# Performance work log

Hardware: AMD Instinct MI355X
Metric: run time of the kernel (lower is better)

The kernel has to match this reference:

```python
import jax, jax.numpy as jnp
import numpy as np

SQRT_DK = jnp.sqrt(jnp.float32(128.0))
BN_EPS = 1e-5


def setup_inputs() -> dict:
    key = jax.random.key(0)
    ks = jax.random.split(key, 12)
    B, C, F, Fp, K, O, DK = 4, 64, 20000, 10000, 16, 128, 128
    fea = jax.random.normal(ks[0], (B, C, F), dtype=jnp.float32)
    ring_n = jax.random.randint(ks[1], (B, Fp, K), 0, F, dtype=jnp.int64)
    pool_idx = jnp.sort(jax.random.randint(ks[2], (Fp,), 0, F, dtype=jnp.int64))
    pos_embed = jnp.zeros((1, 1, 1), dtype=jnp.float32)
    s = 1.0 / np.sqrt(C)
    Wk = jax.random.uniform(ks[3], (DK, C), jnp.float32, -s, s)
    bk = jax.random.uniform(ks[4], (DK,), jnp.float32, -s, s)
    Wq = jax.random.uniform(ks[5], (DK, C), jnp.float32, -s, s)
    bq = jax.random.uniform(ks[6], (DK,), jnp.float32, -s, s)
    Wc = jax.random.uniform(ks[7], (O, C), jnp.float32, -s, s)
    bc = jax.random.uniform(ks[8], (O,), jnp.float32, -s, s)
    gamma = jnp.ones((O,), jnp.float32)
    beta = jnp.zeros((O,), jnp.float32)
    return {"fea": fea, "ring_n": ring_n, "pool_idx": pool_idx, "pos_embed": pos_embed,
            "Wk": Wk, "bk": bk, "Wq": Wq, "bq": bq, "Wc": Wc, "bc": bc,
            "gamma": gamma, "beta": beta}


def _gather_neighbors(fea, ring_n):
    # fea: [B,C,F], ring_n: [B,Fp,K] -> [B,C,Fp,K]
    return jax.vmap(lambda f, r: f[:, r])(fea, ring_n)


def reference(fea, ring_n, pool_idx, pos_embed, Wk, bk, Wq, bq, Wc, bc, gamma, beta):
    # neighbor gather along face dim
    neighbor_fea = _gather_neighbors(fea, ring_n)            # [B,C,Fp,K]
    self_fea = fea[:, :, pool_idx][..., None]                # [B,C,Fp,1]
    cat = jnp.concatenate([self_fea, neighbor_fea], axis=3)  # [B,C,Fp,K+1]
    # per-face key (self only) and per-neighbor query (Linear4D over channel dim)
    keyv = jnp.einsum('bcfk,oc->bofk', self_fea, Wk) + bk[None, :, None, None]  # [B,128,Fp,1]
    query = jnp.einsum('bcfk,oc->bofk', cat, Wq) + bq[None, :, None, None]       # [B,128,Fp,K+1]
    att = jnp.sum(keyv * query, axis=1, keepdims=True) / SQRT_DK                 # [B,1,Fp,K+1]
    att = jax.nn.softmax(att, axis=3)
    agg = jnp.sum(cat * att, axis=3)                                             # [B,C,Fp]
    # concat_mlp: 1x1 conv + BatchNorm1d (training-mode batch stats) + ReLU
    y = jnp.einsum('bcf,oc->bof', agg, Wc) + bc[None, :, None]                   # [B,O,Fp]
    mean = jnp.mean(y, axis=(0, 2), keepdims=True)
    var = jnp.var(y, axis=(0, 2), keepdims=True)
    y = (y - mean) * jax.lax.rsqrt(var + BN_EPS)
    y = y * gamma[None, :, None] + beta[None, :, None]
    return jax.nn.relu(y)
```

## Files before the change

### kernel.cpp

```cpp
#include <hip/hip_runtime.h>

#define F_ALL 20000
#define FP    10000
#define BB    4
#define KK    16
#define OO    128
#define NFACE 40000
#define NBLK  625

#define WS_FEAT 0
#define WS_AGG  (BB*F_ALL*64)
#define WS_GP   (WS_AGG + NFACE*64)
#define WS_SAP  (WS_GP + NBLK*4096)
#define WS_MT   (WS_SAP + NBLK*64)
#define WS_V0   (WS_MT + 4096)
#define WS_G    (WS_V0 + 64)
#define WS_SUMA (WS_G + 4096)
#define WS_SC   (WS_SUMA + 64)
#define WS_SH   (WS_SC + 128)

template<int CTRL>
__device__ __forceinline__ float dpp_add(float x) {
    return x + __int_as_float(__builtin_amdgcn_update_dpp(0, __float_as_int(x), CTRL, 0xF, 0xF, true));
}
__device__ __forceinline__ float sum16(float x) {
    x = dpp_add<0x121>(x);
    x = dpp_add<0x122>(x);
    x = dpp_add<0x124>(x);
    x = dpp_add<0x128>(x);
    return x;
}

__device__ __forceinline__ int swz_tile(int bid) {
    int q = bid & 7, s = bid >> 3;
    return (q == 0) ? s : (79 + (q - 1) * 78 + s);
}

__global__ __launch_bounds__(256) void k_pre(const float* __restrict__ fea,
                                             const float* __restrict__ Wk,
                                             const float* __restrict__ bk,
                                             const float* __restrict__ Wq,
                                             float* __restrict__ ws) {
    __shared__ float tile[64][65];
    int tid = threadIdx.x;
    if (blockIdx.x < 1252) {
        int bb = blockIdx.x / 313;
        int tb = blockIdx.x % 313;
        int fbase = tb * 64;
        int x  = tid & 63;
        int y0 = tid >> 6;
        int f = fbase + x;
        float* feaT = ws + WS_FEAT;
        if (f < F_ALL) {
#pragma unroll
            for (int i = 0; i < 16; i++) {
                int c = y0 + i * 4;
                tile[c][x] = fea[((long)bb * 64 + c) * F_ALL + f];
            }
        }
        __syncthreads();
#pragma unroll
        for (int i = 0; i < 16; i++) {
            int fr = y0 + i * 4;
            int ff = fbase + fr;
            if (ff < F_ALL)
                feaT[((long)bb * F_ALL + ff) * 64 + x] = tile[x][fr];
        }
    } else {
        int idx = (blockIdx.x - 1252) * 256 + tid;
        int j = idx >> 6, i = idx & 63;
        float acc = 0.f;
#pragma unroll 8
        for (int o = 0; o < 128; o++) acc += Wq[o * 64 + i] * Wk[o * 64 + j];
        ws[WS_MT + idx] = acc;
        if (blockIdx.x == 1252 && tid < 64) {
            float a = 0.f;
            for (int o = 0; o < 128; o++) a += Wq[o * 64 + tid] * bk[o];
            ws[WS_V0 + tid] = a;
            ws[WS_SUMA + tid] = 0.f;
        }
    }
}

__global__ __launch_bounds__(256) void k_attn(const int* __restrict__ ring,
                                              const int* __restrict__ pool,
                                              float* __restrict__ ws) {
    __shared__ __align__(16) float lds[12608];
    float* At = lds;
    float* Sf = lds + 4096;
    float* U  = lds + 8256;
    int tid = threadIdx.x;
    int tilei = swz_tile(blockIdx.x);
    int fbase = tilei * 64;
    const float* feaT = ws + WS_FEAT;
    const float scale = 0.08838834764831845f;

    for (int i = tid; i < 4096; i += 256) At[i] = ws[WS_MT + i];
    {
        int r = tid >> 2;
        int face = fbase + r;
        int b = face / FP;
        int p = pool[face - b * FP];
        const float* src = feaT + ((long)(b * F_ALL + p)) * 64;
        int off = (tid & 3) * 4;
#pragma unroll
        for (int it = 0; it < 4; it++, off += 16) {
            float4 v = *(const float4*)(src + off);
            Sf[r * 65 + off + 0] = v.x;
            Sf[r * 65 + off + 1] = v.y;
            Sf[r * 65 + off + 2] = v.z;
            Sf[r * 65 + off + 3] = v.w;
        }
    }
    __syncthreads();

    int ti = tid & 15, tj = tid >> 4;
    {
        int f0 = ti * 4, o0 = tj * 4;
        float4 v0 = *(const float4*)&ws[WS_V0 + o0];
        float acc[4][4];
#pragma unroll
        for (int a = 0; a < 4; a++) {
            acc[a][0] = v0.x; acc[a][1] = v0.y; acc[a][2] = v0.z; acc[a][3] = v0.w;
        }
        for (int j = 0; j < 64; j++) {
            float4 wv = *(const float4*)&At[j * 64 + o0];
#pragma unroll
            for (int a = 0; a < 4; a++) {
                float av = Sf[(f0 + a) * 65 + j];
                acc[a][0] += av * wv.x;
                acc[a][1] += av * wv.y;
                acc[a][2] += av * wv.z;
                acc[a][3] += av * wv.w;
            }
        }
#pragma unroll
        for (int a = 0; a < 4; a++)
            *(float4*)&U[(f0 + a) * 68 + o0] =
                make_float4(acc[a][0], acc[a][1], acc[a][2], acc[a][3]);
    }
    __syncthreads();

    int lane = tid & 63;
    int il = lane & 15, c4 = il * 4;
    float4 a_res[4];
    for (int it = 0; it < 4; it++) {
        int fl = (tid >> 4) + it * 16;
        int face = fbase + fl;
        int b = face / FP;
        const float* fb = feaT + ((long)b * F_ALL) * 64 + c4;

        float4 sf = make_float4(Sf[fl * 65 + c4], Sf[fl * 65 + c4 + 1],
                                Sf[fl * 65 + c4 + 2], Sf[fl * 65 + c4 + 3]);
        float4 u = *(const float4*)&U[fl * 68 + c4];

        int rv = ring[face * KK + il];
        float4 nv[KK];
#pragma unroll
        for (int k = 0; k < KK; k++) {
            int rk = __shfl(rv, (lane & 48) | k, 64);
            nv[k] = *(const float4*)(fb + (long)rk * 64);
        }

        float l[KK + 1];
        l[0] = sum16(u.x * sf.x + u.y * sf.y + u.z * sf.z + u.w * sf.w) * scale;
#pragma unroll
        for (int k = 0; k < KK; k++)
            l[k + 1] = sum16(u.x * nv[k].x + u.y * nv[k].y + u.z * nv[k].z + u.w * nv[k].w) * scale;

        float m = l[0];
#pragma unroll
        for (int k = 1; k <= KK; k++) m = fmaxf(m, l[k]);
        float den = 0.f;
#pragma unroll
        for (int k = 0; k <= KK; k++) { l[k] = __expf(l[k] - m); den += l[k]; }
        float inv = 1.0f / den;

        float4 a;
        a.x = l[0] * sf.x; a.y = l[0] * sf.y; a.z = l[0] * sf.z; a.w = l[0] * sf.w;
#pragma unroll
        for (int k = 0; k < KK; k++) {
            a.x += l[k + 1] * nv[k].x;
            a.y += l[k + 1] * nv[k].y;
            a.z += l[k + 1] * nv[k].z;
            a.w += l[k + 1] * nv[k].w;
        }
        a.x *= inv; a.y *= inv; a.z *= inv; a.w *= inv;
        a_res[it] = a;
        *(float4*)&ws[WS_AGG + (long)face * 64 + c4] = a;
    }
    __syncthreads();
    float* Ag = lds;
#pragma unroll
    for (int it = 0; it < 4; it++) {
        int fl = (tid >> 4) + it * 16;
        *(float4*)&Ag[fl * 64 + c4] = a_res[it];
    }
    __syncthreads();

    float acc[4][4];
#pragma unroll
    for (int a = 0; a < 4; a++)
#pragma unroll
        for (int b = 0; b < 4; b++) acc[a][b] = 0.f;
    float gacc[4] = {0.f, 0.f, 0.f, 0.f};
#pragma unroll 4
    for (int f = 0; f < 64; f++) {
        float4 av = *(const float4*)&Ag[f * 64 + ti * 4];
        float4 bv = *(const float4*)&Ag[f * 64 + tj * 4];
        float avv[4] = {av.x, av.y, av.z, av.w};
        float bvv[4] = {bv.x, bv.y, bv.z, bv.w};
#pragma unroll
        for (int a = 0; a < 4; a++) {
#pragma unroll
            for (int b = 0; b < 4; b++) acc[a][b] += avv[a] * bvv[b];
            gacc[a] += avv[a];
        }
    }
    float* gp = ws + WS_GP;
#pragma unroll
    for (int a = 0; a < 4; a++)
        *(float4*)&gp[(long)tilei * 4096 + (ti * 4 + a) * 64 + tj * 4] =
            make_float4(acc[a][0], acc[a][1], acc[a][2], acc[a][3]);
    if (tj == 0)
        *(float4*)&ws[WS_SAP + tilei * 64 + ti * 4] =
            make_float4(gacc[0], gacc[1], gacc[2], gacc[3]);
}

__global__ __launch_bounds__(256) void k_gsum(float* __restrict__ ws) {
    __shared__ float red[256];
    int t = threadIdx.x;
    if (blockIdx.x < 256) {
        const float* gp = ws + WS_GP;
        int e16 = blockIdx.x * 16;
        int e = t & 15, c = t >> 4;
        int p0 = c * 40;
        int p1 = p0 + 40; if (p1 > NBLK) p1 = NBLK;
        float s0 = 0.f, s1 = 0.f, s2 = 0.f, s3 = 0.f;
        int p = p0;
        for (; p + 4 <= p1; p += 4) {
            s0 += gp[(long)(p + 0) * 4096 + e16 + e];
            s1 += gp[(long)(p + 1) * 4096 + e16 + e];
            s2 += gp[(long)(p + 2) * 4096 + e16 + e];
            s3 += gp[(long)(p + 3) * 4096 + e16 + e];
        }
        for (; p < p1; p++) s0 += gp[(long)p * 4096 + e16 + e];
        red[t] = (s0 + s1) + (s2 + s3);
        __syncthreads();
        if (t < 16) {
            float s = 0.f;
#pragma unroll
            for (int cc = 0; cc < 16; cc++) s += red[cc * 16 + t];
            ws[WS_G + e16 + t] = s;
        }
    } else {
        const float* sap = ws + WS_SAP;
        int bq = blockIdx.x - 256;
        int e = t & 63, c = t >> 6;
        int pidx = bq * 4 + c;
        int p0 = pidx * 40;
        int p1 = p0 + 40; if (p1 > NBLK) p1 = NBLK;
        float s0 = 0.f, s1 = 0.f, s2 = 0.f, s3 = 0.f;
        int p = p0;
        for (; p + 4 <= p1; p += 4) {
            s0 += sap[(p + 0) * 64 + e];
            s1 += sap[(p + 1) * 64 + e];
            s2 += sap[(p + 2) * 64 + e];
            s3 += sap[(p + 3) * 64 + e];
        }
        for (; p < p1; p++) s0 += sap[p * 64 + e];
        red[t] = (s0 + s1) + (s2 + s3);
        __syncthreads();
        if (t < 64) {
            float tot = red[t] + red[t + 64] + red[t + 128] + red[t + 192];
            atomicAdd(&ws[WS_SUMA + t], tot);
        }
    }
}

__global__ __launch_bounds__(256) void k_stats(const float* __restrict__ Wc,
                                               const float* __restrict__ bc,
                                               const float* __restrict__ gamma,
                                               const float* __restrict__ beta,
                                               float* __restrict__ ws) {
    __shared__ float Gs[4096];
    __shared__ float gs[64];
    __shared__ float qs[256];
    int tid = threadIdx.x;
    for (int i = tid; i < 4096; i += 256) Gs[i] = ws[WS_G + i];
    if (tid < 64) gs[tid] = ws[WS_SUMA + tid];
    __syncthreads();

    int o = tid & 127, h = tid >> 7;
    float w[64];
#pragma unroll
    for (int q = 0; q < 16; q++) {
        float4 t = *(const float4*)&Wc[o * 64 + q * 4];
        w[q * 4 + 0] = t.x; w[q * 4 + 1] = t.y; w[q * 4 + 2] = t.z; w[q * 4 + 3] = t.w;
    }
    float qp = 0.f;
    for (int i = h * 32; i < h * 32 + 32; i++) {
        float t = 0.f;
#pragma unroll
        for (int j = 0; j < 64; j++) t += Gs[i * 64 + j] * w[j];
        qp += Wc[o * 64 + i] * t;
    }
    qs[tid] = qp;
    __syncthreads();
    if (h == 0) {
        const float invN = 1.0f / (float)NFACE;
        float qform = qs[o] + qs[o + 128];
        float md = 0.f;
#pragma unroll
        for (int j = 0; j < 64; j++) md += gs[j] * w[j];
        float bco = bc[o];
        float mean = md * invN + bco;
        float ey2  = (qform + 2.f * bco * md) * invN + bco * bco;
        float var  = ey2 - mean * mean;
        float sc   = gamma[o] * rsqrtf(var + 1e-5f);
        ws[WS_SC + o] = sc;
        ws[WS_SH + o] = beta[o] + (bco - mean) * sc;
    }
}

__global__ __launch_bounds__(256) void k_out(const float* __restrict__ Wc,
                                             const float* __restrict__ ws,
                                             float* __restrict__ out) {
    __shared__ __align__(16) float WcT[64 * 132];
    __shared__ __align__(16) float AgT[64 * 68];
    const float* agg = ws + WS_AGG;
    int tid = threadIdx.x;
    int fbase = blockIdx.x * 64;
    for (int i = tid; i < 128 * 64; i += 256) {
        int o = i >> 6, j = i & 63;
        WcT[j * 132 + o] = Wc[i];
    }
    for (int i = tid; i < 64 * 64; i += 256) {
        int f = i >> 6, j = i & 63;
        AgT[j * 68 + f] = agg[((long)(fbase + f)) * 64 + j];
    }
    __syncthreads();

    int tx = tid & 15, ty = tid >> 4;
    float acc[8][4];
#pragma unroll
    for (int a = 0; a < 8; a++)
#pragma unroll
        for (int b = 0; b < 4; b++) acc[a][b] = 0.f;

    for (int j = 0; j < 64; j++) {
        float4 w0 = *(const float4*)&WcT[j * 132 + ty * 8];
        float4 w1 = *(const float4*)&WcT[j * 132 + ty * 8 + 4];
        float4 a0 = *(const float4*)&AgT[j * 68 + tx * 4];
        float wv[8] = {w0.x, w0.y, w0.z, w0.w, w1.x, w1.y, w1.z, w1.w};
        float av[4] = {a0.x, a0.y, a0.z, a0.w};
#pragma unroll
        for (int oi = 0; oi < 8; oi++)
#pragma unroll
            for (int fi = 0; fi < 4; fi++) acc[oi][fi] += wv[oi] * av[fi];
    }

    int fg0 = fbase + tx * 4;
    int b   = fg0 / FP;
    int fp0 = fg0 - b * FP;
#pragma unroll
    for (int oi = 0; oi < 8; oi++) {
        int o = ty * 8 + oi;
        float sc = ws[WS_SC + o];
        float sh = ws[WS_SH + o];
        float4 v;
        v.x = fmaxf(acc[oi][0] * sc + sh, 0.f);
        v.y = fmaxf(acc[oi][1] * sc + sh, 0.f);
        v.z = fmaxf(acc[oi][2] * sc + sh, 0.f);
        v.w = fmaxf(acc[oi][3] * sc + sh, 0.f);
        *(float4*)&out[((long)(b * OO + o)) * FP + fp0] = v;
    }
}

extern "C" void kernel_launch(void* const* d_in, const int* in_sizes, int n_in,
                              void* d_out, int out_size, void* d_ws, size_t ws_size,
                              hipStream_t stream) {
    const float* fea  = (const float*)d_in[0];
    const int*   ring = (const int*)d_in[1];
    const int*   pool = (const int*)d_in[2];
    const float* Wk = (const float*)d_in[4];
    const float* bk = (const float*)d_in[5];
    const float* Wq = (const float*)d_in[6];
    const float* Wc = (const float*)d_in[8];
    const float* bc = (const float*)d_in[9];
    const float* gamma = (const float*)d_in[10];
    const float* beta  = (const float*)d_in[11];

    float* out = (float*)d_out;
    float* ws  = (float*)d_ws;

    k_pre  <<<1268, 256, 0, stream>>>(fea, Wk, bk, Wq, ws);
    k_attn <<<NBLK, 256, 0, stream>>>(ring, pool, ws);
    k_gsum <<<260,  256, 0, stream>>>(ws);
    k_stats<<<1,    256, 0, stream>>>(Wc, bc, gamma, beta, ws);
    k_out  <<<NBLK, 256, 0, stream>>>(Wc, ws, out);
}
```

Measured before the change: 168.1 us.

## Compute key projection in registers and use chunked online softmax in attention

The k_attn kernel no longer stages the 64x64 Wq^T Wk matrix and the per-face U tile in LDS. Each thread now computes its own U values directly from global memory (cache-resident) in the layout used by the attention loop, which removes one barrier and shrinks LDS from about 50KB to about 16KB, aiming at higher occupancy. The neighbor gather and softmax are split into two chunks of 8 using an online-softmax rescale, reducing live registers for the gathered vectors. The trade-off is more global/L1 loads for the matrix and fewer loads in flight per chunk, which may hurt latency hiding for the random gather.

```diff
diff --git a/kernel.cpp b/kernel.cpp
--- a/kernel.cpp
+++ b/kernel.cpp
@@ -85,17 +85,15 @@
 __global__ __launch_bounds__(256) void k_attn(const int* __restrict__ ring,
                                               const int* __restrict__ pool,
                                               float* __restrict__ ws) {
-    __shared__ __align__(16) float lds[12608];
-    float* At = lds;
-    float* Sf = lds + 4096;
-    float* U  = lds + 8256;
+    __shared__ __align__(16) float lds[4160];
+    float* Sf = lds;
     int tid = threadIdx.x;
     int tilei = swz_tile(blockIdx.x);
     int fbase = tilei * 64;
     const float* feaT = ws + WS_FEAT;
+    const float* MTg  = ws + WS_MT;
     const float scale = 0.08838834764831845f;
 
-    for (int i = tid; i < 4096; i += 256) At[i] = ws[WS_MT + i];
     {
         int r = tid >> 2;
         int face = fbase + r;
@@ -114,78 +112,77 @@
     }
     __syncthreads();
 
-    int ti = tid & 15, tj = tid >> 4;
-    {
-        int f0 = ti * 4, o0 = tj * 4;
-        float4 v0 = *(const float4*)&ws[WS_V0 + o0];
-        float acc[4][4];
-#pragma unroll
-        for (int a = 0; a < 4; a++) {
-            acc[a][0] = v0.x; acc[a][1] = v0.y; acc[a][2] = v0.z; acc[a][3] = v0.w;
-        }
-        for (int j = 0; j < 64; j++) {
-            float4 wv = *(const float4*)&At[j * 64 + o0];
-#pragma unroll
-            for (int a = 0; a < 4; a++) {
-                float av = Sf[(f0 + a) * 65 + j];
-                acc[a][0] += av * wv.x;
-                acc[a][1] += av * wv.y;
-                acc[a][2] += av * wv.z;
-                acc[a][3] += av * wv.w;
-            }
-        }
-#pragma unroll
-        for (int a = 0; a < 4; a++)
-            *(float4*)&U[(f0 + a) * 68 + o0] =
-                make_float4(acc[a][0], acc[a][1], acc[a][2], acc[a][3]);
-    }
-    __syncthreads();
-
     int lane = tid & 63;
     int il = lane & 15, c4 = il * 4;
+    int f0 = tid >> 4;
+
+    float4 u[4];
+    {
+        float4 v0 = *(const float4*)&ws[WS_V0 + c4];
+        u[0] = v0; u[1] = v0; u[2] = v0; u[3] = v0;
+#pragma unroll 8
+        for (int j = 0; j < 64; j++) {
+            float4 m4 = *(const float4*)&MTg[j * 64 + c4];
+            float a0 = Sf[(f0     ) * 65 + j];
+            float a1 = Sf[(f0 + 16) * 65 + j];
+            float a2 = Sf[(f0 + 32) * 65 + j];
+            float a3 = Sf[(f0 + 48) * 65 + j];
+            u[0].x += m4.x * a0; u[0].y += m4.y * a0; u[0].z += m4.z * a0; u[0].w += m4.w * a0;
+            u[1].x += m4.x * a1; u[1].y += m4.y * a1; u[1].z += m4.z * a1; u[1].w += m4.w * a1;
+            u[2].x += m4.x * a2; u[2].y += m4.y * a2; u[2].z += m4.z * a2; u[2].w += m4.w * a2;
+            u[3].x += m4.x * a3; u[3].y += m4.y * a3; u[3].z += m4.z * a3; u[3].w += m4.w * a3;
+        }
+    }
+
     float4 a_res[4];
+#pragma unroll
     for (int it = 0; it < 4; it++) {
-        int fl = (tid >> 4) + it * 16;
+        int fl = f0 + it * 16;
         int face = fbase + fl;
         int b = face / FP;
         const float* fb = feaT + ((long)b * F_ALL) * 64 + c4;
 
         float4 sf = make_float4(Sf[fl * 65 + c4], Sf[fl * 65 + c4 + 1],
                                 Sf[fl * 65 + c4 + 2], Sf[fl * 65 + c4 + 3]);
-        float4 u = *(const float4*)&U[fl * 68 + c4];
-
+        float4 uu = u[it];
         int rv = ring[face * KK + il];
-        float4 nv[KK];
-#pragma unroll
-        for (int k = 0; k < KK; k++) {
-            int rk = __shfl(rv, (lane & 48) | k, 64);
-            nv[k] = *(const float4*)(fb + (long)rk * 64);
-        }
-
-        float l[KK + 1];
-        l[0] = sum16(u.x * sf.x + u.y * sf.y + u.z * sf.z + u.w * sf.w) * scale;
-#pragma unroll
-        for (int k = 0; k < KK; k++)
-            l[k + 1] = sum16(u.x * nv[k].x + u.y * nv[k].y + u.z * nv[k].z + u.w * nv[k].w) * scale;
-
-        float m = l[0];
-#pragma unroll
-        for (int k = 1; k <= KK; k++) m = fmaxf(m, l[k]);
-        float den = 0.f;
-#pragma unroll
-        for (int k = 0; k <= KK; k++) { l[k] = __expf(l[k] - m); den += l[k]; }
+
+        float m = sum16(uu.x * sf.x + uu.y * sf.y + uu.z * sf.z + uu.w * sf.w) * scale;
+        float den = 1.f;
+        float4 acc = sf;
+#pragma unroll
+        for (int ch = 0; ch < 2; ch++) {
+            float4 nv[8];
+#pragma unroll
+            for (int k = 0; k < 8; k++) {
+                int rk = __shfl(rv, (lane & 48) | (ch * 8 + k), 64);
+                nv[k] = *(const float4*)(fb + (long)rk * 64);
+            }
+            float l[8];
+#pragma unroll
+            for (int k = 0; k < 8; k++)
+                l[k] = sum16(uu.x * nv[k].x + uu.y * nv[k].y +
+                             uu.z * nv[k].z + uu.w * nv[k].w) * scale;
+            float cm = l[0];
+#pragma unroll
+            for (int k = 1; k < 8; k++) cm = fmaxf(cm, l[k]);
+            float nm = fmaxf(m, cm);
+            float rs = __expf(m - nm);
+            den *= rs;
+            acc.x *= rs; acc.y *= rs; acc.z *= rs; acc.w *= rs;
+            m = nm;
+#pragma unroll
+            for (int k = 0; k < 8; k++) {
+                float e = __expf(l[k] - m);
+                den += e;
+                acc.x += e * nv[k].x;
+                acc.y += e * nv[k].y;
+                acc.z += e * nv[k].z;
+                acc.w += e * nv[k].w;
+            }
+        }
         float inv = 1.0f / den;
-
-        float4 a;
-        a.x = l[0] * sf.x; a.y = l[0] * sf.y; a.z = l[0] * sf.z; a.w = l[0] * sf.w;
-#pragma unroll
-        for (int k = 0; k < KK; k++) {
-            a.x += l[k + 1] * nv[k].x;
-            a.y += l[k + 1] * nv[k].y;
-            a.z += l[k + 1] * nv[k].z;
-            a.w += l[k + 1] * nv[k].w;
-        }
-        a.x *= inv; a.y *= inv; a.z *= inv; a.w *= inv;
+        float4 a = make_float4(acc.x * inv, acc.y * inv, acc.z * inv, acc.w * inv);
         a_res[it] = a;
         *(float4*)&ws[WS_AGG + (long)face * 64 + c4] = a;
     }
@@ -193,11 +190,12 @@
     float* Ag = lds;
 #pragma unroll
     for (int it = 0; it < 4; it++) {
-        int fl = (tid >> 4) + it * 16;
+        int fl = f0 + it * 16;
         *(float4*)&Ag[fl * 64 + c4] = a_res[it];
     }
     __syncthreads();
 
+    int ti = tid & 15, tj = tid >> 4;
     float acc[4][4];
 #pragma unroll
     for (int a = 0; a < 4; a++)
```

Measured after the change: 165.7 us. About the same (-1.4%).
